# Kernel tuning notes

Hardware: AMD Instinct MI355X
Metric: run time of the kernel (lower is better)

## Reference

```python
import jax, jax.numpy as jnp
import numpy as np

DIM = 512
HEADS = 16
KS = 5  # side_dwconv


def setup_inputs() -> dict:
    key = jax.random.key(0)
    ks = jax.random.split(key, 6)
    B, H, W = 8, 32, 32
    x = jax.random.normal(ks[0], (B, H, W, DIM), dtype=jnp.float32)
    # qkv linear (no bias): torch Linear weight [3C, C]
    w_qkv = jax.random.normal(ks[1], (3 * DIM, DIM), dtype=jnp.float32) * (1.0 / np.sqrt(DIM))
    # output projection
    w_proj = jax.random.normal(ks[2], (DIM, DIM), dtype=jnp.float32) * (1.0 / np.sqrt(DIM))
    b_proj = jax.random.normal(ks[3], (DIM,), dtype=jnp.float32) * 0.01
    # depthwise conv kernel: torch Conv2d(groups=dim) weight [C, 1, k, k]
    w_lepe = jax.random.normal(ks[4], (DIM, 1, KS, KS), dtype=jnp.float32) * (1.0 / KS)
    b_lepe = jax.random.normal(ks[5], (DIM,), dtype=jnp.float32) * 0.01
    return {"x": x, "w_qkv": w_qkv, "w_proj": w_proj, "b_proj": b_proj,
            "w_lepe": w_lepe, "b_lepe": b_lepe}


def _depthwise_conv(x_nchw, w, b):
    # x: [B, C, H, W], w: [C, 1, k, k] (OIHW with feature_group_count=C)
    out = jax.lax.conv_general_dilated(
        x_nchw, w,
        window_strides=(1, 1),
        padding=[(KS // 2, KS // 2), (KS // 2, KS // 2)],
        dimension_numbers=("NCHW", "OIHW", "NCHW"),
        feature_group_count=x_nchw.shape[1],
    )
    return out + b[None, :, None, None]


def reference(x, w_qkv, w_proj, b_proj, w_lepe, b_lepe):
    B, H, W, C = x.shape
    N = H * W
    hd = C // HEADS
    scale = hd ** (-0.5)

    xt = x.reshape(B, N, C)  # n (h w) c

    qkv = xt @ w_qkv.T  # [B, N, 3C]
    qkv = qkv.reshape(B, N, 3, HEADS, hd).transpose(2, 0, 3, 1, 4)  # [3, B, h, N, d]
    q, k, v = qkv[0], qkv[1], qkv[2]

    # LePE depthwise conv positional encoding
    lepe = _depthwise_conv(xt.reshape(B, H, W, C).transpose(0, 3, 1, 2), w_lepe, b_lepe)
    lepe = lepe.transpose(0, 2, 3, 1).reshape(B, N, C)

    attn = jnp.einsum("bhnd,bhmd->bhnm", q, k) * scale
    attn = jax.nn.softmax(attn, axis=-1)
    out = jnp.einsum("bhnm,bhmd->bhnd", attn, v)
    out = out.transpose(0, 2, 1, 3).reshape(B, N, C)

    out = out + lepe
    out = out @ w_proj.T + b_proj
    return out.reshape(B, H, W, C)
```

## Files before the change

### kernel.cpp

```cpp
#include <hip/hip_runtime.h>
#include <hip/hip_bf16.h>

typedef unsigned int u32;
typedef unsigned short u16;
typedef __attribute__((ext_vector_type(8))) short bfrag;
typedef __attribute__((ext_vector_type(4))) float ffrag;

__device__ __forceinline__ float bf2f(u16 h) { u32 v = ((u32)h) << 16; return __builtin_bit_cast(float, v); }
__device__ __forceinline__ u16 f2bf_bits(float f) {
  u32 x = __builtin_bit_cast(u32, f);
  x += 0x7FFFu + ((x >> 16) & 1u);
  return (u16)(x >> 16);
}
__device__ __forceinline__ u32 pack2f(float a, float b) {
  __hip_bfloat162 h = __float22bfloat162_rn(float2{a, b});
  u32 r;
  __builtin_memcpy(&r, &h, 4);
  return r;
}
__device__ __forceinline__ float fast_exp2(float x) {
#if __has_builtin(__builtin_amdgcn_exp2f)
  return __builtin_amdgcn_exp2f(x);
#else
  return __expf(x * 0.6931471805599453f);
#endif
}

__global__ __launch_bounds__(256) void cvt_bf16(const float* __restrict__ X,
                                                const float* __restrict__ Wq,
                                                const float* __restrict__ Wp,
                                                u16* __restrict__ xb,
                                                u16* __restrict__ wqb,
                                                u16* __restrict__ wpb) {
  const int idx = blockIdx.x * 256 + threadIdx.x;
  const int NX = 1048576;
  const int NQ = 196608;
  const float* src;
  u16* dst;
  int off;
  if (idx < NX)            { src = X;  dst = xb;  off = idx; }
  else if (idx < NX + NQ)  { src = Wq; dst = wqb; off = idx - NX; }
  else                     { src = Wp; dst = wpb; off = idx - NX - NQ; }
  float4 v = ((const float4*)src)[off];
  uint2 r;
  r.x = pack2f(v.x, v.y);
  r.y = pack2f(v.z, v.w);
  ((uint2*)dst)[off] = r;
}

__global__ __launch_bounds__(256) void qkv_gemm(const u16* __restrict__ Xb,
                                                const u16* __restrict__ Wqb,
                                                u16* __restrict__ qb,
                                                u16* __restrict__ kb,
                                                u16* __restrict__ vb) {
  __shared__ u16 As[128][40];
  __shared__ u16 Bs[128][40];
  const int tid = threadIdx.x;
  const int lane = tid & 63;
  const int w = tid >> 6;
  const int wr = w >> 1, wc = w & 1;
  const int lrow = lane & 15, quad = lane >> 4;
  const int bm0 = blockIdx.x * 128;
  const int bn0 = blockIdx.y * 128;
  const int lr = tid >> 1;
  const int lc = (tid & 1) * 16;

  ffrag acc[4][4];
#pragma unroll
  for (int i = 0; i < 4; i++)
#pragma unroll
    for (int j = 0; j < 4; j++) acc[i][j] = (ffrag){0.f, 0.f, 0.f, 0.f};

  const u16* arow = Xb + (bm0 + lr) * 512 + lc;
  const u16* brow = Wqb + (bn0 + lr) * 512 + lc;
  uint4 a0 = ((const uint4*)arow)[0], a1 = ((const uint4*)arow)[1];
  uint4 b0 = ((const uint4*)brow)[0], b1 = ((const uint4*)brow)[1];

  for (int k0 = 0; k0 < 512; k0 += 32) {
    __syncthreads();
    *(uint4*)(&As[lr][lc])     = a0;
    *(uint4*)(&As[lr][lc + 8]) = a1;
    *(uint4*)(&Bs[lr][lc])     = b0;
    *(uint4*)(&Bs[lr][lc + 8]) = b1;
    __syncthreads();
    if (k0 + 32 < 512) {
      const uint4* apn = (const uint4*)(arow + k0 + 32);
      const uint4* bpn = (const uint4*)(brow + k0 + 32);
      a0 = apn[0]; a1 = apn[1];
      b0 = bpn[0]; b1 = bpn[1];
    }
    bfrag af[4], bf[4];
#pragma unroll
    for (int i = 0; i < 4; i++) af[i] = *(const bfrag*)(&As[wr * 64 + i * 16 + lrow][quad * 8]);
#pragma unroll
    for (int j = 0; j < 4; j++) bf[j] = *(const bfrag*)(&Bs[wc * 64 + j * 16 + lrow][quad * 8]);
#pragma unroll
    for (int i = 0; i < 4; i++)
#pragma unroll
      for (int j = 0; j < 4; j++)
        acc[i][j] = __builtin_amdgcn_mfma_f32_16x16x32_bf16(af[i], bf[j], acc[i][j], 0, 0, 0);
  }

#pragma unroll
  for (int i = 0; i < 4; i++)
#pragma unroll
    for (int j = 0; j < 4; j++) {
      int jj = bn0 + wc * 64 + j * 16 + lrow;
      int which = jj >> 9, rem = jj & 511;
      int h = rem >> 5, d = rem & 31;
      u16* dst = (which == 0) ? qb : (which == 1) ? kb : vb;
#pragma unroll
      for (int r = 0; r < 4; r++) {
        int m = bm0 + wr * 64 + i * 16 + quad * 4 + r;
        int pair = ((m >> 10) << 4) + h;
        int n = m & 1023;
        dst[(pair * 1024 + n) * 32 + d] = f2bf_bits(acc[i][j][r]);
      }
    }
}

__global__ __launch_bounds__(256) void lepe_conv(const float* __restrict__ X,
                                                 const float* __restrict__ Wl,
                                                 const float* __restrict__ bl,
                                                 u16* __restrict__ out) {
  __shared__ float Wls[512 * 25];
  const int tid = threadIdx.x;
  const int c = tid * 2;
  const int y = blockIdx.x;
  const int b = blockIdx.y;
  const int x0 = blockIdx.z * 16;

  {
    const float2* src = (const float2*)Wl;
    float2* dst = (float2*)Wls;
#pragma unroll
    for (int i = 0; i < 25; i++) dst[tid + i * 256] = src[tid + i * 256];
  }
  __syncthreads();

  float w0[25], w1[25];
#pragma unroll
  for (int t = 0; t < 25; t++) {
    w0[t] = Wls[c * 25 + t];
    w1[t] = Wls[(c + 1) * 25 + t];
  }
  const float2 bias = *(const float2*)(bl + c);

  const float* rowp[5];
  bool rowv[5];
#pragma unroll
  for (int r = 0; r < 5; r++) {
    int yy = y + r - 2;
    rowv[r] = (yy >= 0) && (yy < 32);
    rowp[r] = X + ((b * 32 + (rowv[r] ? yy : 0)) * 32) * 512 + c;
  }

  float2 win[5][5];
#pragma unroll
  for (int rel = -2; rel <= 1; rel++) {
    const int slot = ((rel % 5) + 5) % 5;
    const int xcol = x0 + rel;
    const bool xv = (xcol >= 0) && (xcol < 32);
#pragma unroll
    for (int r = 0; r < 5; r++)
      win[r][slot] = (xv && rowv[r]) ? *(const float2*)(rowp[r] + xcol * 512)
                                     : float2{0.f, 0.f};
  }

#pragma unroll
  for (int xi = 0; xi < 16; xi++) {
    {
      const int slot = (xi + 2) % 5;
      const int xcol = x0 + xi + 2;
      const bool xv = (xcol < 32);
#pragma unroll
      for (int r = 0; r < 5; r++)
        win[r][slot] = (xv && rowv[r]) ? *(const float2*)(rowp[r] + xcol * 512)
                                       : float2{0.f, 0.f};
    }
    float a0 = bias.x, a1 = bias.y;
#pragma unroll
    for (int ky = 0; ky < 5; ky++)
#pragma unroll
      for (int kx = 0; kx < 5; kx++) {
        const int rel = xi - 2 + kx;
        const int slot = ((rel % 5) + 5) % 5;
        const float2 v = win[ky][slot];
        const int t = ky * 5 + kx;
        a0 = fmaf(v.x, w0[t], a0);
        a1 = fmaf(v.y, w1[t], a1);
      }
    const int sp = (b * 32 + y) * 32 + x0 + xi;
    *(u32*)(out + sp * 512 + c) = pack2f(a0, a1);
  }
}

__global__ __launch_bounds__(512, 4) void attn_mfma(const u16* __restrict__ qb,
                                                    const u16* __restrict__ kb,
                                                    const u16* __restrict__ vb,
                                                    const u16* __restrict__ lp,
                                                    u16* __restrict__ ao) {
  __shared__ u32 Vt[32][132];
  __shared__ u32 Ps[8][16][20];
  const int tid = threadIdx.x, lane = tid & 63, w = tid >> 6;
  const int quad = lane >> 4, m16 = lane & 15;
  const int pair = blockIdx.x >> 2;
  const int quarter = blockIdx.x & 3;
  const int b = pair >> 4, h = pair & 15;

  const int wq0 = quarter * 256 + w * 32;
  bfrag qf[2];
#pragma unroll
  for (int i = 0; i < 2; i++) {
    int row = wq0 + i * 16 + m16;
    qf[i] = *(const bfrag*)(qb + (pair * 1024 + row) * 32 + quad * 8);
  }

  const float SC2 = 0.25503448540239605f;
  const float SHIFT2 = 11.541560327111707f;
  const u16* kbase = kb + pair * 32768;
  const u16* vbase = vb + pair * 32768;

  bfrag onesf;
#pragma unroll
  for (int e = 0; e < 8; e++) onesf[e] = (short)0x3F80;

  ffrag oacc[2][2], sacc[2];
#pragma unroll
  for (int i = 0; i < 2; i++) {
    oacc[i][0] = (ffrag){0.f, 0.f, 0.f, 0.f};
    oacc[i][1] = (ffrag){0.f, 0.f, 0.f, 0.f};
    sacc[i]    = (ffrag){0.f, 0.f, 0.f, 0.f};
  }

  const int pp = tid & 127;
  const int vq = tid >> 7;
  const int vg = pp >> 4, vt = pp & 15;
  const int jbase = vg * 32 + vt;
  uint4 svl = *(const uint4*)(vbase + jbase * 32 + vq * 8);
  uint4 svh = *(const uint4*)(vbase + (jbase + 16) * 32 + vq * 8);

  bfrag kf0n = *(const bfrag*)(kbase + (m16) * 32 + quad * 8);
  bfrag kf1n = *(const bfrag*)(kbase + (16 + m16) * 32 + quad * 8);

  for (int jc = 0; jc < 1024; jc += 256) {
    __syncthreads();
    {
      u32 lw[4] = {svl.x, svl.y, svl.z, svl.w};
      u32 hw[4] = {svh.x, svh.y, svh.z, svh.w};
#pragma unroll
      for (int e = 0; e < 4; e++) {
        int d0 = vq * 8 + e * 2;
        Vt[d0][pp]     = (lw[e] & 0xFFFFu) | (hw[e] << 16);
        Vt[d0 + 1][pp] = (lw[e] >> 16) | (hw[e] & 0xFFFF0000u);
      }
    }
    __syncthreads();
    if (jc + 256 < 1024) {
      int jlo = jc + 256 + jbase;
      svl = *(const uint4*)(vbase + jlo * 32 + vq * 8);
      svh = *(const uint4*)(vbase + (jlo + 16) * 32 + vq * 8);
    }

    for (int j0 = 0; j0 < 256; j0 += 32) {
      const int g0 = j0 >> 5;
      bfrag kf0 = kf0n, kf1 = kf1n;
      {
        const int jn = jc + j0 + 32;
        kf0n = *(const bfrag*)(kbase + (jn + m16) * 32 + quad * 8);
        kf1n = *(const bfrag*)(kbase + (jn + 16 + m16) * 32 + quad * 8);
      }
      ffrag s[2][2];
      __builtin_amdgcn_s_setprio(1);
#pragma unroll
      for (int i = 0; i < 2; i++) {
        s[i][0] = __builtin_amdgcn_mfma_f32_16x16x32_bf16(qf[i], kf0, (ffrag){0.f,0.f,0.f,0.f}, 0, 0, 0);
        s[i][1] = __builtin_amdgcn_mfma_f32_16x16x32_bf16(qf[i], kf1, (ffrag){0.f,0.f,0.f,0.f}, 0, 0, 0);
      }
      __builtin_amdgcn_s_setprio(0);
      bfrag vf0 = *(const bfrag*)(&Vt[m16][g0 * 16 + quad * 4]);
      bfrag vf1 = *(const bfrag*)(&Vt[16 + m16][g0 * 16 + quad * 4]);

#pragma unroll
      for (int i = 0; i < 2; i++) {
#pragma unroll
        for (int r = 0; r < 4; r++) {
          float p0 = fast_exp2(fmaf(s[i][0][r], SC2, -SHIFT2));
          float p1 = fast_exp2(fmaf(s[i][1][r], SC2, -SHIFT2));
          Ps[w][quad * 4 + r][m16] =
              (__builtin_bit_cast(u32, p0) >> 16) | (__builtin_bit_cast(u32, p1) & 0xFFFF0000u);
        }
        bfrag pf = *(const bfrag*)(&Ps[w][m16][quad * 4]);
        __builtin_amdgcn_s_setprio(1);
        oacc[i][0] = __builtin_amdgcn_mfma_f32_16x16x32_bf16(pf, vf0, oacc[i][0], 0, 0, 0);
        oacc[i][1] = __builtin_amdgcn_mfma_f32_16x16x32_bf16(pf, vf1, oacc[i][1], 0, 0, 0);
        sacc[i]    = __builtin_amdgcn_mfma_f32_16x16x32_bf16(pf, onesf, sacc[i], 0, 0, 0);
        __builtin_amdgcn_s_setprio(0);
      }
    }
  }

#pragma unroll
  for (int i = 0; i < 2; i++) {
    float inv[4];
#pragma unroll
    for (int r = 0; r < 4; r++) inv[r] = 1.0f / sacc[i][r];
#pragma unroll
    for (int jd = 0; jd < 2; jd++)
#pragma unroll
      for (int r = 0; r < 4; r++) {
        int row = wq0 + i * 16 + quad * 4 + r;
        int col = jd * 16 + m16;
        int o = (b * 1024 + row) * 512 + h * 32 + col;
        float val = fmaf(oacc[i][jd][r], inv[r], bf2f(lp[o]));
        ao[o] = f2bf_bits(val);
      }
  }
}

__global__ __launch_bounds__(256) void proj_gemm(const u16* __restrict__ Y,
                                                 const u16* __restrict__ Wpb,
                                                 const float* __restrict__ bp,
                                                 float* __restrict__ out) {
  __shared__ u16 As[128][40];
  __shared__ u16 Bs[64][40];
  const int tid = threadIdx.x;
  const int lane = tid & 63;
  const int w = tid >> 6;
  const int wr = w >> 1, wc = w & 1;
  const int lrow = lane & 15, quad = lane >> 4;
  const int bm0 = blockIdx.x * 128;
  const int bn0 = blockIdx.y * 64;
  const int lr = tid >> 1;
  const int lc = (tid & 1) * 16;
  const int br = tid >> 2;
  const int bc = (tid & 3) * 8;

  ffrag acc[4][2];
#pragma unroll
  for (int i = 0; i < 4; i++)
#pragma unroll
    for (int j = 0; j < 2; j++) acc[i][j] = (ffrag){0.f, 0.f, 0.f, 0.f};

  const u16* arow = Y + (bm0 + lr) * 512 + lc;
  const u16* brow = Wpb + (bn0 + br) * 512 + bc;
  uint4 a0 = ((const uint4*)arow)[0], a1 = ((const uint4*)arow)[1];
  uint4 b0 = *(const uint4*)brow;

  for (int k0 = 0; k0 < 512; k0 += 32) {
    __syncthreads();
    *(uint4*)(&As[lr][lc])     = a0;
    *(uint4*)(&As[lr][lc + 8]) = a1;
    *(uint4*)(&Bs[br][bc])     = b0;
    __syncthreads();
    if (k0 + 32 < 512) {
      const uint4* apn = (const uint4*)(arow + k0 + 32);
      a0 = apn[0]; a1 = apn[1];
      b0 = *(const uint4*)(brow + k0 + 32);
    }
    bfrag af[4], bf[2];
#pragma unroll
    for (int i = 0; i < 4; i++) af[i] = *(const bfrag*)(&As[wr * 64 + i * 16 + lrow][quad * 8]);
#pragma unroll
    for (int j = 0; j < 2; j++) bf[j] = *(const bfrag*)(&Bs[wc * 32 + j * 16 + lrow][quad * 8]);
#pragma unroll
    for (int i = 0; i < 4; i++)
#pragma unroll
      for (int j = 0; j < 2; j++)
        acc[i][j] = __builtin_amdgcn_mfma_f32_16x16x32_bf16(af[i], bf[j], acc[i][j], 0, 0, 0);
  }

#pragma unroll
  for (int i = 0; i < 4; i++)
#pragma unroll
    for (int j = 0; j < 2; j++) {
      int jj = bn0 + wc * 32 + j * 16 + lrow;
      float bias = bp[jj];
#pragma unroll
      for (int r = 0; r < 4; r++) {
        int m = bm0 + wr * 64 + i * 16 + quad * 4 + r;
        out[m * 512 + jj] = acc[i][j][r] + bias;
      }
    }
}

extern "C" void kernel_launch(void* const* d_in, const int* in_sizes, int n_in,
                              void* d_out, int out_size, void* d_ws, size_t ws_size,
                              hipStream_t stream) {
  const float* x      = (const float*)d_in[0];
  const float* w_qkv  = (const float*)d_in[1];
  const float* w_proj = (const float*)d_in[2];
  const float* b_proj = (const float*)d_in[3];
  const float* w_lepe = (const float*)d_in[4];
  const float* b_lepe = (const float*)d_in[5];
  float* out = (float*)d_out;

  char* ws = (char*)d_ws;
  const size_t SEG = 8388608;
  u16* qb  = (u16*)(ws + 0 * SEG);
  u16* kb  = (u16*)(ws + 1 * SEG);
  u16* vb  = (u16*)(ws + 2 * SEG);
  u16* ao  = (u16*)(ws + 3 * SEG);
  u16* lp  = (u16*)(ws + 4 * SEG);
  u16* xb  = (u16*)(ws + 5 * SEG);
  u16* wqb = (u16*)(ws + 6 * SEG);
  u16* wpb = (u16*)(ws + 6 * SEG + 1572864);

  hipLaunchKernelGGL(cvt_bf16, dim3(5120), dim3(256), 0, stream, x, w_qkv, w_proj, xb, wqb, wpb);
  hipLaunchKernelGGL(qkv_gemm, dim3(64, 12), dim3(256), 0, stream, xb, wqb, qb, kb, vb);
  hipLaunchKernelGGL(lepe_conv, dim3(32, 8, 2), dim3(256), 0, stream, x, w_lepe, b_lepe, lp);
  hipLaunchKernelGGL(attn_mfma, dim3(512), dim3(512), 0, stream, qb, kb, vb, lp, ao);
  hipLaunchKernelGGL(proj_gemm, dim3(64, 8), dim3(256), 0, stream, ao, wpb, b_proj, out);
}
```

Measured before the change: 158.6 us.

## Fuse x bf16 conversion into LePE conv; compute S transposed to skip LDS round-trip

```diff
diff --git a/kernel.cpp b/kernel.cpp
--- a/kernel.cpp
+++ b/kernel.cpp
@@ -5,6 +5,7 @@
 typedef unsigned short u16;
 typedef __attribute__((ext_vector_type(8))) short bfrag;
 typedef __attribute__((ext_vector_type(4))) float ffrag;
+typedef __attribute__((ext_vector_type(4))) u32 u32x4;
 
 __device__ __forceinline__ float bf2f(u16 h) { u32 v = ((u32)h) << 16; return __builtin_bit_cast(float, v); }
 __device__ __forceinline__ u16 f2bf_bits(float f) {
@@ -26,21 +27,17 @@
 #endif
 }
 
-__global__ __launch_bounds__(256) void cvt_bf16(const float* __restrict__ X,
-                                                const float* __restrict__ Wq,
-                                                const float* __restrict__ Wp,
-                                                u16* __restrict__ xb,
-                                                u16* __restrict__ wqb,
-                                                u16* __restrict__ wpb) {
+__global__ __launch_bounds__(256) void cvt_w(const float* __restrict__ Wq,
+                                             const float* __restrict__ Wp,
+                                             u16* __restrict__ wqb,
+                                             u16* __restrict__ wpb) {
   const int idx = blockIdx.x * 256 + threadIdx.x;
-  const int NX = 1048576;
   const int NQ = 196608;
   const float* src;
   u16* dst;
   int off;
-  if (idx < NX)            { src = X;  dst = xb;  off = idx; }
-  else if (idx < NX + NQ)  { src = Wq; dst = wqb; off = idx - NX; }
-  else                     { src = Wp; dst = wpb; off = idx - NX - NQ; }
+  if (idx < NQ) { src = Wq; dst = wqb; off = idx; }
+  else          { src = Wp; dst = wpb; off = idx - NQ; }
   float4 v = ((const float4*)src)[off];
   uint2 r;
   r.x = pack2f(v.x, v.y);
@@ -122,7 +119,8 @@
 __global__ __launch_bounds__(256) void lepe_conv(const float* __restrict__ X,
                                                  const float* __restrict__ Wl,
                                                  const float* __restrict__ bl,
-                                                 u16* __restrict__ out) {
+                                                 u16* __restrict__ out,
+                                                 u16* __restrict__ xb) {
   __shared__ float Wls[512 * 25];
   const int tid = threadIdx.x;
   const int c = tid * 2;
@@ -192,6 +190,8 @@
       }
     const int sp = (b * 32 + y) * 32 + x0 + xi;
     *(u32*)(out + sp * 512 + c) = pack2f(a0, a1);
+    const float2 ctr = win[2][xi % 5];
+    *(u32*)(xb + sp * 512 + c) = pack2f(ctr.x, ctr.y);
   }
 }
 
@@ -201,7 +201,6 @@
                                                     const u16* __restrict__ lp,
                                                     u16* __restrict__ ao) {
   __shared__ u32 Vt[32][132];
-  __shared__ u32 Ps[8][16][20];
   const int tid = threadIdx.x, lane = tid & 63, w = tid >> 6;
   const int quad = lane >> 4, m16 = lane & 15;
   const int pair = blockIdx.x >> 2;
@@ -221,16 +220,12 @@
   const u16* kbase = kb + pair * 32768;
   const u16* vbase = vb + pair * 32768;
 
-  bfrag onesf;
-#pragma unroll
-  for (int e = 0; e < 8; e++) onesf[e] = (short)0x3F80;
-
-  ffrag oacc[2][2], sacc[2];
+  ffrag oacc[2][2];
+  float lsum[2] = {0.f, 0.f};
 #pragma unroll
   for (int i = 0; i < 2; i++) {
     oacc[i][0] = (ffrag){0.f, 0.f, 0.f, 0.f};
     oacc[i][1] = (ffrag){0.f, 0.f, 0.f, 0.f};
-    sacc[i]    = (ffrag){0.f, 0.f, 0.f, 0.f};
   }
 
   const int pp = tid & 127;
@@ -270,31 +265,29 @@
         kf0n = *(const bfrag*)(kbase + (jn + m16) * 32 + quad * 8);
         kf1n = *(const bfrag*)(kbase + (jn + 16 + m16) * 32 + quad * 8);
       }
-      ffrag s[2][2];
-      __builtin_amdgcn_s_setprio(1);
-#pragma unroll
-      for (int i = 0; i < 2; i++) {
-        s[i][0] = __builtin_amdgcn_mfma_f32_16x16x32_bf16(qf[i], kf0, (ffrag){0.f,0.f,0.f,0.f}, 0, 0, 0);
-        s[i][1] = __builtin_amdgcn_mfma_f32_16x16x32_bf16(qf[i], kf1, (ffrag){0.f,0.f,0.f,0.f}, 0, 0, 0);
-      }
-      __builtin_amdgcn_s_setprio(0);
       bfrag vf0 = *(const bfrag*)(&Vt[m16][g0 * 16 + quad * 4]);
       bfrag vf1 = *(const bfrag*)(&Vt[16 + m16][g0 * 16 + quad * 4]);
 
 #pragma unroll
       for (int i = 0; i < 2; i++) {
+        __builtin_amdgcn_s_setprio(1);
+        ffrag s0 = __builtin_amdgcn_mfma_f32_16x16x32_bf16(kf0, qf[i], (ffrag){0.f,0.f,0.f,0.f}, 0, 0, 0);
+        ffrag s1 = __builtin_amdgcn_mfma_f32_16x16x32_bf16(kf1, qf[i], (ffrag){0.f,0.f,0.f,0.f}, 0, 0, 0);
+        __builtin_amdgcn_s_setprio(0);
+        u32x4 paw;
+        float acc0 = 0.f, acc1 = 0.f;
 #pragma unroll
         for (int r = 0; r < 4; r++) {
-          float p0 = fast_exp2(fmaf(s[i][0][r], SC2, -SHIFT2));
-          float p1 = fast_exp2(fmaf(s[i][1][r], SC2, -SHIFT2));
-          Ps[w][quad * 4 + r][m16] =
-              (__builtin_bit_cast(u32, p0) >> 16) | (__builtin_bit_cast(u32, p1) & 0xFFFF0000u);
+          float p0 = fast_exp2(fmaf(s0[r], SC2, -SHIFT2));
+          float p1 = fast_exp2(fmaf(s1[r], SC2, -SHIFT2));
+          paw[r] = pack2f(p0, p1);
+          acc0 += p0; acc1 += p1;
         }
-        bfrag pf = *(const bfrag*)(&Ps[w][m16][quad * 4]);
+        lsum[i] += acc0 + acc1;
+        bfrag pa = __builtin_bit_cast(bfrag, paw);
         __builtin_amdgcn_s_setprio(1);
-        oacc[i][0] = __builtin_amdgcn_mfma_f32_16x16x32_bf16(pf, vf0, oacc[i][0], 0, 0, 0);
-        oacc[i][1] = __builtin_amdgcn_mfma_f32_16x16x32_bf16(pf, vf1, oacc[i][1], 0, 0, 0);
-        sacc[i]    = __builtin_amdgcn_mfma_f32_16x16x32_bf16(pf, onesf, sacc[i], 0, 0, 0);
+        oacc[i][0] = __builtin_amdgcn_mfma_f32_16x16x32_bf16(pa, vf0, oacc[i][0], 0, 0, 0);
+        oacc[i][1] = __builtin_amdgcn_mfma_f32_16x16x32_bf16(pa, vf1, oacc[i][1], 0, 0, 0);
         __builtin_amdgcn_s_setprio(0);
       }
     }
@@ -302,9 +295,15 @@
 
 #pragma unroll
   for (int i = 0; i < 2; i++) {
+    float l = lsum[i];
+    l += __shfl_xor(l, 16);
+    l += __shfl_xor(l, 32);
     float inv[4];
 #pragma unroll
-    for (int r = 0; r < 4; r++) inv[r] = 1.0f / sacc[i][r];
+    for (int r = 0; r < 4; r++) {
+      int src = (lane & 0x30) | (quad * 4 + r);
+      inv[r] = 1.0f / __shfl(l, src);
+    }
 #pragma unroll
     for (int jd = 0; jd < 2; jd++)
 #pragma unroll
@@ -406,9 +405,9 @@
   u16* wqb = (u16*)(ws + 6 * SEG);
   u16* wpb = (u16*)(ws + 6 * SEG + 1572864);
 
-  hipLaunchKernelGGL(cvt_bf16, dim3(5120), dim3(256), 0, stream, x, w_qkv, w_proj, xb, wqb, wpb);
+  hipLaunchKernelGGL(cvt_w, dim3(1024), dim3(256), 0, stream, w_qkv, w_proj, wqb, wpb);
+  hipLaunchKernelGGL(lepe_conv, dim3(32, 8, 2), dim3(256), 0, stream, x, w_lepe, b_lepe, lp, xb);
   hipLaunchKernelGGL(qkv_gemm, dim3(64, 12), dim3(256), 0, stream, xb, wqb, qb, kb, vb);
-  hipLaunchKernelGGL(lepe_conv, dim3(32, 8, 2), dim3(256), 0, stream, x, w_lepe, b_lepe, lp);
   hipLaunchKernelGGL(attn_mfma, dim3(512), dim3(512), 0, stream, qb, kb, vb, lp, ao);
   hipLaunchKernelGGL(proj_gemm, dim3(64, 8), dim3(256), 0, stream, ao, wpb, b_proj, out);
 }
```

Measured after the change: 165.2 us. 4.1% more time.
